# Optimization experiments

Hardware: AMD Instinct MI355X
Metric: run time of the kernel (lower is better)

Reference implementation:

```python
import jax, jax.numpy as jnp
import numpy as np

B, S, H, HEADS = 2, 2048, 1024, 16
KD = H // HEADS          # key_dim = 64
VDIM = 2 * H             # double_v_dim
HD = VDIM // HEADS       # head_size = 128
EPS = 1e-5


def _rotate_every_two(x):
    x1 = x[..., ::2]
    x2 = x[..., 1::2]
    return jnp.stack((-x2, x1), axis=-1).reshape(x.shape)


def _theta_shift(x, sin, cos):
    return x * cos + _rotate_every_two(x) * sin


def setup_inputs() -> dict:
    key = jax.random.key(0)
    ks = jax.random.split(key, 8)
    x = jax.random.normal(ks[0], (B, S, H), dtype=jnp.float32)
    # RoPE-style angles over key_dim, each frequency repeated twice
    half = jnp.arange(KD // 2, dtype=jnp.float32)
    angle = 1.0 / (10000.0 ** (half / (KD // 2)))
    angle = jnp.repeat(angle, 2)                      # [KD]
    pos = jnp.arange(S, dtype=jnp.float32)[:, None]   # [S,1]
    sin = jnp.sin(pos * angle[None, :])               # [S,KD]
    cos = jnp.cos(pos * angle[None, :])
    # per-head exponential decay mask (RetNet)
    decay = 1.0 - 2.0 ** (-5.0 - jnp.arange(HEADS, dtype=jnp.float32))  # [heads]
    i = jnp.arange(S, dtype=jnp.float32)[:, None]
    j = jnp.arange(S, dtype=jnp.float32)[None, :]
    diff = i - j                                       # [S,S]
    logd = jnp.log(decay)[:, None, None]               # [heads,1,1]
    mask = jnp.where(diff[None] >= 0, jnp.exp(logd * diff[None]), 0.0).astype(jnp.float32)
    gain = 0.02
    Wq = gain * jax.random.normal(ks[1], (H, H), dtype=jnp.float32)
    Wk = gain * jax.random.normal(ks[2], (H, H), dtype=jnp.float32)
    Wv = gain * jax.random.normal(ks[3], (VDIM, H), dtype=jnp.float32)
    Wg = gain * jax.random.normal(ks[4], (VDIM, H), dtype=jnp.float32)
    Wo = gain * jax.random.normal(ks[5], (H, VDIM), dtype=jnp.float32)
    return {"x": x, "sin": sin, "cos": cos, "mask": mask,
            "Wq": Wq, "Wk": Wk, "Wv": Wv, "Wg": Wg, "Wo": Wo}


def reference(x, sin, cos, mask, Wq, Wk, Wv, Wg, Wo):
    b, s, h = x.shape
    heads = mask.shape[0]
    kd = h // heads
    vdim = Wv.shape[0]
    hd = vdim // heads
    scaling = kd ** -0.5

    q = jnp.einsum('bsh,oh->bso', x, Wq)
    k = jnp.einsum('bsh,oh->bso', x, Wk) * scaling
    v = jnp.einsum('bsh,oh->bso', x, Wv)
    g = jnp.einsum('bsh,oh->bso', x, Wg)

    q = q.reshape(b, s, heads, kd).transpose(0, 2, 1, 3)  # [b,h,s,kd]
    k = k.reshape(b, s, heads, kd).transpose(0, 2, 1, 3)
    qr = _theta_shift(q, sin, cos)
    kr = _theta_shift(k, sin, cos)

    vr = v.reshape(b, s, heads, hd).transpose(0, 2, 1, 3)  # [b,h,s,hd]

    qk = jnp.einsum('bhsk,bhtk->bhst', qr, kr) * mask      # [b,h,s,s]
    denom = jnp.maximum(jnp.abs(jax.lax.stop_gradient(qk).sum(-1, keepdims=True)), 1.0)
    qk = qk / denom

    out = jnp.einsum('bhst,bhtd->bhsd', qk, vr)            # [b,h,s,hd]
    out = out.transpose(0, 2, 1, 3)                        # [b,s,h,hd]
    # RMSNorm over head_size, no affine, eps=1e-5
    out = out * jax.lax.rsqrt(jnp.mean(out * out, axis=-1, keepdims=True) + EPS)
    out = out.reshape(b, s, heads * hd)                    # [b,s,vdim]
    out = (g * jax.nn.sigmoid(g)) * out                    # swish gate
    return jnp.einsum('bsv,ov->bso', out, Wo)
```

## Files before the change

kernel.cpp:

```cpp
#include <hip/hip_runtime.h>

typedef _Float16 f16;
typedef _Float16 f16x2 __attribute__((ext_vector_type(2)));
typedef _Float16 f16x4 __attribute__((ext_vector_type(4)));
typedef _Float16 f16x8 __attribute__((ext_vector_type(8)));
typedef float f32x4 __attribute__((ext_vector_type(4)));

#define MFMA_16x16x32(a, b, c) __builtin_amdgcn_mfma_f32_16x16x32_f16((a), (b), (c), 0, 0, 0)


__device__ __forceinline__ void async_ld16(const void* g, void* l) {
  __builtin_amdgcn_global_load_lds((const __attribute__((address_space(1))) unsigned int*)g,
                                   (__attribute__((address_space(3))) unsigned int*)l,
                                   16, 0, 0);
}

__global__ void k_cast_all(const float* __restrict__ x, const float* __restrict__ Wq,
                           const float* __restrict__ Wk, const float* __restrict__ Wv,
                           const float* __restrict__ Wg, const float* __restrict__ Wo,
                           f16* __restrict__ xh, f16* __restrict__ W1h, f16* __restrict__ Woh) {
  size_t u = ((size_t)blockIdx.x * 256 + threadIdx.x) * 4;
  const float* src;
  f16* dst;
  float sc = 1.0f;
  if (u < 4194304) {
    src = x + u; dst = xh + u;
  } else if (u < 10485760) {
    size_t idx = u - 4194304;
    int row = (int)(idx >> 10), col = (int)(idx & 1023);
    if (row < 1024)      { src = Wq + (size_t)row * 1024 + col; }
    else if (row < 2048) { src = Wk + (size_t)(row - 1024) * 1024 + col; sc = 0.125f; }
    else if (row < 4096) { src = Wv + (size_t)(row - 2048) * 1024 + col; }
    else                 { src = Wg + (size_t)(row - 4096) * 1024 + col; }
    dst = W1h + idx;
  } else {
    size_t idx = u - 10485760;
    src = Wo + idx; dst = Woh + idx;
  }
  float4 v = *(const float4*)src;
  f16x4 r = { (f16)(v.x * sc), (f16)(v.y * sc), (f16)(v.z * sc), (f16)(v.w * sc) };
  *(f16x4*)dst = r;
}

template <int NT, typename OutT>
__global__ __launch_bounds__(256, 2)
void k_gemm_bt(const f16* __restrict__ A, const f16* __restrict__ Bw,
               OutT* __restrict__ C, int M, int N, int K) {
  __shared__ f16 As[128 * 64];
  __shared__ f16 Bs[NT * 64];
  constexpr int NR = NT / 16;
  const int tid = threadIdx.x;
  const int lane = tid & 63, w = tid >> 6;
  const int quad = lane >> 4, rm = lane & 15;
  const int mt = blockIdx.y, nt = blockIdx.x;
  const f16* Ab = A + (size_t)mt * 128 * K;
  const f16* Bb = Bw + (size_t)nt * NT * K;
  f32x4 acc[2][NR] = {};

  const int sr = lane >> 3;
  const int sc8 = (lane & 7) * 8;

  for (int k0 = 0; k0 < K; k0 += 64) {
    __syncthreads();
#pragma unroll
    for (int p = 0; p < 4; ++p) {
      int br = w * 32 + p * 8;
      async_ld16(Ab + (size_t)(br + sr) * K + k0 + sc8, &As[br * 64]);
    }
#pragma unroll
    for (int p = 0; p < NT / 32; ++p) {
      int br = w * (NT / 4) + p * 8;
      async_ld16(Bb + (size_t)(br + sr) * K + k0 + sc8, &Bs[br * 64]);
    }
    __syncthreads();
#pragma unroll
    for (int kk = 0; kk < 64; kk += 32) {
      const int ko = kk + quad * 8;
      f16x8 a0 = *(const f16x8*)(&As[(w * 32 + rm) * 64 + ko]);
      f16x8 a1 = *(const f16x8*)(&As[(w * 32 + 16 + rm) * 64 + ko]);
#pragma unroll
      for (int n = 0; n < NR; ++n) {
        f16x8 bf = *(const f16x8*)(&Bs[(n * 16 + rm) * 64 + ko]);
        acc[0][n] = MFMA_16x16x32(a0, bf, acc[0][n]);
        acc[1][n] = MFMA_16x16x32(a1, bf, acc[1][n]);
      }
    }
  }
#pragma unroll
  for (int m = 0; m < 2; ++m)
#pragma unroll
    for (int n = 0; n < NR; ++n)
#pragma unroll
      for (int r = 0; r < 4; ++r) {
        int row = mt * 128 + w * 32 + m * 16 + quad * 4 + r;
        int col = nt * NT + n * 16 + rm;
        C[(size_t)row * N + col] = (OutT)acc[m][n][r];
      }
}

__global__ void k_rope(f16* __restrict__ qkvg, const float* __restrict__ sinp,
                       const float* __restrict__ cosp) {
  int u = blockIdx.x * 256 + threadIdx.x;
  int row = u >> 10;
  int col = (u & 1023) * 2;
  int s = row & 2047;
  int d = col & 63;
  f16x2* p = (f16x2*)(qkvg + (size_t)row * 6144 + col);
  f16x2 xv = *p;
  float xe = (float)xv[0], xo = (float)xv[1];
  float se = sinp[s * 64 + d], so = sinp[s * 64 + d + 1];
  float ce = cosp[s * 64 + d], co = cosp[s * 64 + d + 1];
  f16x2 r = { (f16)(xe * ce - xo * se), (f16)(xo * co + xe * so) };
  *p = r;
}

__device__ __forceinline__ int off136(int d) { return d * 136 + ((d >> 3) << 3); }

__global__ __launch_bounds__(256, 2)
void k_state(const f16* __restrict__ qkvg, float* __restrict__ Sws, float* __restrict__ skws) {
  __shared__ f16 Kt[8752];
  __shared__ f16 Vt[17520];
  __shared__ float skbuf[4][64];
  const int tid = threadIdx.x;
  const int lane = tid & 63, w = tid >> 6;
  const int quad = lane >> 4, rm = lane & 15;
  const int c = blockIdx.x, h = blockIdx.y, b = blockIdx.z;
  const int bh = b * 16 + h;
  const size_t ld = 6144;
  const f16* base = qkvg + (size_t)b * 2048 * ld + (size_t)c * 128 * ld;
  const float logd = logf(1.0f - exp2f(-5.0f - (float)h));

#pragma unroll
  for (int p = 0; p < 4; ++p) {
    int tau = p * 32 + (tid >> 3);
    int kd0 = (tid & 7) * 8;
    f16x8 kv = *(const f16x8*)(base + (size_t)tau * ld + 1024 + h * 64 + kd0);
    float g = expf(logd * (float)(127 - tau));
#pragma unroll
    for (int j = 0; j < 8; ++j) Kt[off136(kd0 + j) + tau] = (f16)((float)kv[j] * g);
  }
#pragma unroll
  for (int p = 0; p < 8; ++p) {
    int tau = p * 16 + (tid >> 4);
    int d0 = (tid & 15) * 8;
    f16x8 vv = *(const f16x8*)(base + (size_t)tau * ld + 2048 + h * 128 + d0);
#pragma unroll
    for (int j = 0; j < 8; ++j) Vt[off136(d0 + j) + tau] = vv[j];
  }
  __syncthreads();

  f32x4 acc[2][4] = {};
#pragma unroll
  for (int kf = 0; kf < 4; ++kf) {
    int k0 = kf * 32 + quad * 8;
    f16x8 av[2];
#pragma unroll
    for (int mm = 0; mm < 2; ++mm)
      av[mm] = *(const f16x8*)(&Vt[off136(w * 32 + mm * 16 + rm) + k0]);
#pragma unroll
    for (int n = 0; n < 4; ++n) {
      f16x8 bk = *(const f16x8*)(&Kt[off136(n * 16 + rm) + k0]);
#pragma unroll
      for (int mm = 0; mm < 2; ++mm) acc[mm][n] = MFMA_16x16x32(av[mm], bk, acc[mm][n]);
    }
  }
  float* Sout = Sws + ((size_t)c * 32 + bh) * 8192;
#pragma unroll
  for (int mm = 0; mm < 2; ++mm)
#pragma unroll
    for (int n = 0; n < 4; ++n)
#pragma unroll
      for (int r = 0; r < 4; ++r)
        Sout[(w * 32 + mm * 16 + quad * 4 + r) * 64 + n * 16 + rm] = acc[mm][n][r];

  {
    int kd = tid & 63;
    float p = 0.f;
    for (int tau = w * 32; tau < w * 32 + 32; ++tau) p += (float)Kt[off136(kd) + tau];
    skbuf[w][kd] = p;
  }
  __syncthreads();
  if (tid < 64) {
    float s = skbuf[0][tid] + skbuf[1][tid] + skbuf[2][tid] + skbuf[3][tid];
    skws[((size_t)c * 32 + bh) * 64 + tid] = s;
  }
}

__global__ __launch_bounds__(256, 2)
void k_scan(const float* __restrict__ Sws, const float* __restrict__ skws,
            f16* __restrict__ Rtws, float* __restrict__ rktws) {
  const int bh = blockIdx.x;
  const int h = bh & 15;
  const int tid = threadIdx.x;
  const float logd = logf(1.0f - exp2f(-5.0f - (float)h));
  const float gC = expf(logd * 128.0f);
  float R[32];
#pragma unroll
  for (int i = 0; i < 32; ++i) R[i] = 0.f;
  float rk = 0.f;
  for (int c = 0; c < 16; ++c) {
    size_t bs = ((size_t)c * 32 + bh) * 8192;
    f16* rt = Rtws + bs;
    const float* sp = Sws + bs;
#pragma unroll
    for (int i = 0; i < 32; ++i) {
      rt[tid * 32 + i] = (f16)R[i];
      R[i] = gC * R[i] + sp[tid * 32 + i];
    }
    if (tid < 64) {
      size_t ks = ((size_t)c * 32 + bh) * 64 + tid;
      rktws[ks] = rk;
      rk = gC * rk + skws[ks];
    }
  }
}

__device__ __forceinline__ int vt_off(int d) { return d * 40 + (d >> 3) * 8; }

__global__ __launch_bounds__(256, 4)
void k_attn(const f16* __restrict__ qkvg, const f16* __restrict__ Rtws,
            const float* __restrict__ rktws, f16* __restrict__ act) {
  constexpr int LDK = 72;
  constexpr int LDP = 40;
  __shared__ f16 Ks[32 * LDK];
  __shared__ f16 Vt[5240];
  __shared__ f16 Ps[4][16 * LDP];
  const int tid = threadIdx.x;
  const int lane = tid & 63, w = tid >> 6;
  const int quad = lane >> 4, rm = lane & 15;
  int bx = blockIdx.x;
  if (blockIdx.z) bx = 31 - bx;
  const int h = blockIdx.y, b = blockIdx.z;
  const int bh = b * 16 + h;
  const int s_blk = bx * 64;
  const int c = s_blk >> 7;
  const size_t ld = 6144;
  const f16* base = qkvg + (size_t)b * 2048 * ld;
  const float logd = logf(1.0f - exp2f(-5.0f - (float)h));

  f16x8 qa[2];
  {
    int row = s_blk + w * 16 + rm;
#pragma unroll
    for (int kh = 0; kh < 2; ++kh)
      qa[kh] = *(const f16x8*)(base + (size_t)row * ld + h * 64 + kh * 32 + quad * 8);
  }
  int voff[8];
#pragma unroll
  for (int n = 0; n < 8; ++n) voff[n] = vt_off(n * 16 + rm) + quad * 8;

  f32x4 od[8];
#pragma unroll
  for (int n = 0; n < 8; ++n) od[n] = (f32x4){0.f, 0.f, 0.f, 0.f};
  float den[4] = {0.f, 0.f, 0.f, 0.f};

  const int tmax = s_blk + 64;
  for (int t0 = c * 128; t0 < tmax; t0 += 32) {
    __syncthreads();
    {
      int r = tid >> 3, cc = (tid & 7) * 8;
      *(uint4*)(&Ks[r * LDK + cc]) =
          *(const uint4*)(base + (size_t)(t0 + r) * ld + 1024 + h * 64 + cc);
    }
#pragma unroll
    for (int p = 0; p < 2; ++p) {
      int t = p * 16 + (tid >> 4);
      int d0 = (tid & 15) * 8;
      f16x8 v = *(const f16x8*)(base + (size_t)(t0 + t) * ld + 2048 + h * 128 + d0);
#pragma unroll
      for (int j = 0; j < 8; ++j) Vt[vt_off(d0 + j) + t] = v[j];
    }
    __syncthreads();

    f32x4 st[2];
#pragma unroll
    for (int ts = 0; ts < 2; ++ts) st[ts] = (f32x4){0.f, 0.f, 0.f, 0.f};
#pragma unroll
    for (int ts = 0; ts < 2; ++ts) {
      f16x8 bk0 = *(const f16x8*)(&Ks[(ts * 16 + rm) * LDK + quad * 8]);
      f16x8 bk1 = *(const f16x8*)(&Ks[(ts * 16 + rm) * LDK + 32 + quad * 8]);
      st[ts] = MFMA_16x16x32(qa[0], bk0, st[ts]);
      st[ts] = MFMA_16x16x32(qa[1], bk1, st[ts]);
    }
#pragma unroll
    for (int ts = 0; ts < 2; ++ts)
#pragma unroll
      for (int r = 0; r < 4; ++r) {
        int s = s_blk + w * 16 + quad * 4 + r;
        int t = t0 + ts * 16 + rm;
        int diff = s - t;
        float pv = 0.f;
        if (diff >= 0) pv = st[ts][r] * expf(logd * (float)diff);
        den[r] += pv;
        Ps[w][(quad * 4 + r) * LDP + ts * 16 + rm] = (f16)pv;
      }
    __syncthreads();
    f16x8 pa = *(const f16x8*)(&Ps[w][rm * LDP + quad * 8]);
#pragma unroll
    for (int n = 0; n < 8; ++n) {
      f16x8 bv = *(const f16x8*)(&Vt[voff[n]]);
      od[n] = MFMA_16x16x32(pa, bv, od[n]);
    }
  }

  {
    const f16* Rt = Rtws + ((size_t)c * 32 + bh) * 8192;
    float g1 = expf(logd * (float)(s_blk - c * 128 + w * 16 + rm + 1));
    f16x8 qg[2];
#pragma unroll
    for (int kh = 0; kh < 2; ++kh)
#pragma unroll
      for (int j = 0; j < 8; ++j) qg[kh][j] = (f16)((float)qa[kh][j] * g1);
#pragma unroll
    for (int n = 0; n < 8; ++n) {
      f16x8 b0 = *(const f16x8*)(Rt + (size_t)(n * 16 + rm) * 64 + quad * 8);
      f16x8 b1 = *(const f16x8*)(Rt + (size_t)(n * 16 + rm) * 64 + 32 + quad * 8);
      od[n] = MFMA_16x16x32(qg[0], b0, od[n]);
      od[n] = MFMA_16x16x32(qg[1], b1, od[n]);
    }
    const float* rkp = rktws + ((size_t)c * 32 + bh) * 64;
    f16x8 bd0, bd1;
#pragma unroll
    for (int j = 0; j < 8; ++j) {
      bd0[j] = (rm == 0) ? (f16)rkp[quad * 8 + j] : (f16)0.f;
      bd1[j] = (rm == 0) ? (f16)rkp[32 + quad * 8 + j] : (f16)0.f;
    }
    f32x4 sd = (f32x4){0.f, 0.f, 0.f, 0.f};
    sd = MFMA_16x16x32(qg[0], bd0, sd);
    sd = MFMA_16x16x32(qg[1], bd1, sd);
#pragma unroll
    for (int r = 0; r < 4; ++r) den[r] += sd[r];
  }

  float dn[4], rr[4];
#pragma unroll
  for (int r = 0; r < 4; ++r) {
    float d = den[r];
    d += __shfl_xor(d, 1, 16);
    d += __shfl_xor(d, 2, 16);
    d += __shfl_xor(d, 4, 16);
    d += __shfl_xor(d, 8, 16);
    dn[r] = fmaxf(fabsf(d), 1.0f);
  }
  float ssq[4] = {0.f, 0.f, 0.f, 0.f};
#pragma unroll
  for (int n = 0; n < 8; ++n)
#pragma unroll
    for (int r = 0; r < 4; ++r) {
      float o = od[n][r] / dn[r];
      od[n][r] = o;
      ssq[r] += o * o;
    }
#pragma unroll
  for (int r = 0; r < 4; ++r) {
    float s2 = ssq[r];
    s2 += __shfl_xor(s2, 1, 16);
    s2 += __shfl_xor(s2, 2, 16);
    s2 += __shfl_xor(s2, 4, 16);
    s2 += __shfl_xor(s2, 8, 16);
    rr[r] = rsqrtf(s2 * (1.0f / 128.0f) + 1e-5f);
  }
#pragma unroll
  for (int n = 0; n < 8; ++n)
#pragma unroll
    for (int r = 0; r < 4; ++r) {
      int s = s_blk + w * 16 + quad * 4 + r;
      int dcol = n * 16 + rm;
      float g = (float)base[(size_t)s * ld + 4096 + h * 128 + dcol];
      float o = od[n][r] * rr[r];
      float a = (g / (1.0f + expf(-g))) * o;
      act[((size_t)b * 2048 + s) * 2048 + h * 128 + dcol] = (f16)a;
    }
}

extern "C" void kernel_launch(void* const* d_in, const int* in_sizes, int n_in,
                              void* d_out, int out_size, void* d_ws, size_t ws_size,
                              hipStream_t stream) {
  const float* x    = (const float*)d_in[0];
  const float* sinp = (const float*)d_in[1];
  const float* cosp = (const float*)d_in[2];
  const float* Wq = (const float*)d_in[4];
  const float* Wk = (const float*)d_in[5];
  const float* Wv = (const float*)d_in[6];
  const float* Wg = (const float*)d_in[7];
  const float* Wo = (const float*)d_in[8];
  float* out = (float*)d_out;

  char* ws = (char*)d_ws;
  f16* xh     = (f16*)(ws);
  f16* W1h    = (f16*)(ws + 8388608);
  f16* Woh    = (f16*)(ws + 20971520);
  f16* qkvg   = (f16*)(ws + 25165824);
  f16* acth   = (f16*)(ws + 75497472);
  float* Sws  = (float*)(ws + 92274688);
  f16* Rtws   = (f16*)(ws + 109051904);
  float* skws = (float*)(ws + 117440512);
  float* rktws= (float*)(ws + 117571584);

  k_cast_all<<<12288, 256, 0, stream>>>(x, Wq, Wk, Wv, Wg, Wo, xh, W1h, Woh);

  k_gemm_bt<128, f16><<<dim3(48, 32), 256, 0, stream>>>(xh, W1h, qkvg, 4096, 6144, 1024);

  k_rope<<<16384, 256, 0, stream>>>(qkvg, sinp, cosp);

  k_state<<<dim3(16, 16, 2), 256, 0, stream>>>(qkvg, Sws, skws);
  k_scan<<<32, 256, 0, stream>>>(Sws, skws, Rtws, rktws);
  k_attn<<<dim3(32, 16, 2), 256, 0, stream>>>(qkvg, Rtws, rktws, acth);

  k_gemm_bt<64, float><<<dim3(16, 32), 256, 0, stream>>>(acth, Woh, out, 4096, 1024, 2048);
}
```

Measured before the change: 518.8 us.

## Fuse RoPE into QKVG GEMM epilogue, store chunk states in fp16, parallelize scan

Applies the rotary shift inside the projection GEMM epilogue, pairing adjacent columns with a lane shuffle, and removes the separate k_rope pass over q and k. Chunk state matrices are written in fp16 instead of fp32, which halves that workspace traffic. The scan kernel is split across 8 slabs per batch-head with vectorized 4-wide accesses instead of 32 sequential values per thread, giving 256 blocks rather than 32. The costs are some precision loss in the stored states and extra sin/cos loads in the GEMM epilogue.

Measured after the change: 499.2 us. 3.8% less time.

```diff
diff --git a/kernel.cpp b/kernel.cpp
--- a/kernel.cpp
+++ b/kernel.cpp
@@ -42,10 +42,11 @@
   *(f16x4*)dst = r;
 }
 
-template <int NT, typename OutT>
+template <int NT, bool ROPE, typename OutT>
 __global__ __launch_bounds__(256, 2)
 void k_gemm_bt(const f16* __restrict__ A, const f16* __restrict__ Bw,
-               OutT* __restrict__ C, int M, int N, int K) {
+               OutT* __restrict__ C, const float* __restrict__ sinp,
+               const float* __restrict__ cosp, int M, int N, int K) {
   __shared__ f16 As[128 * 64];
   __shared__ f16 Bs[NT * 64];
   constexpr int NR = NT / 16;
@@ -86,6 +87,7 @@
       }
     }
   }
+  const bool rope_tile = ROPE && (nt * NT < 2048);
 #pragma unroll
   for (int m = 0; m < 2; ++m)
 #pragma unroll
@@ -94,30 +96,22 @@
       for (int r = 0; r < 4; ++r) {
         int row = mt * 128 + w * 32 + m * 16 + quad * 4 + r;
         int col = nt * NT + n * 16 + rm;
-        C[(size_t)row * N + col] = (OutT)acc[m][n][r];
+        float val = acc[m][n][r];
+        if (rope_tile) {
+          float par = __shfl_xor(val, 1);
+          int s = row & 2047;
+          int d = col & 63;
+          float sv = sinp[s * 64 + d], cv = cosp[s * 64 + d];
+          val = (col & 1) ? (val * cv + par * sv) : (val * cv - par * sv);
+        }
+        C[(size_t)row * N + col] = (OutT)val;
       }
 }
 
-__global__ void k_rope(f16* __restrict__ qkvg, const float* __restrict__ sinp,
-                       const float* __restrict__ cosp) {
-  int u = blockIdx.x * 256 + threadIdx.x;
-  int row = u >> 10;
-  int col = (u & 1023) * 2;
-  int s = row & 2047;
-  int d = col & 63;
-  f16x2* p = (f16x2*)(qkvg + (size_t)row * 6144 + col);
-  f16x2 xv = *p;
-  float xe = (float)xv[0], xo = (float)xv[1];
-  float se = sinp[s * 64 + d], so = sinp[s * 64 + d + 1];
-  float ce = cosp[s * 64 + d], co = cosp[s * 64 + d + 1];
-  f16x2 r = { (f16)(xe * ce - xo * se), (f16)(xo * co + xe * so) };
-  *p = r;
-}
-
 __device__ __forceinline__ int off136(int d) { return d * 136 + ((d >> 3) << 3); }
 
 __global__ __launch_bounds__(256, 2)
-void k_state(const f16* __restrict__ qkvg, float* __restrict__ Sws, float* __restrict__ skws) {
+void k_state(const f16* __restrict__ qkvg, f16* __restrict__ Sws, float* __restrict__ skws) {
   __shared__ f16 Kt[8752];
   __shared__ f16 Vt[17520];
   __shared__ float skbuf[4][64];
@@ -164,14 +158,14 @@
       for (int mm = 0; mm < 2; ++mm) acc[mm][n] = MFMA_16x16x32(av[mm], bk, acc[mm][n]);
     }
   }
-  float* Sout = Sws + ((size_t)c * 32 + bh) * 8192;
+  f16* Sout = Sws + ((size_t)c * 32 + bh) * 8192;
 #pragma unroll
   for (int mm = 0; mm < 2; ++mm)
 #pragma unroll
     for (int n = 0; n < 4; ++n)
 #pragma unroll
       for (int r = 0; r < 4; ++r)
-        Sout[(w * 32 + mm * 16 + quad * 4 + r) * 64 + n * 16 + rm] = acc[mm][n][r];
+        Sout[(w * 32 + mm * 16 + quad * 4 + r) * 64 + n * 16 + rm] = (f16)acc[mm][n][r];
 
   {
     int kd = tid & 63;
@@ -187,27 +181,27 @@
 }
 
 __global__ __launch_bounds__(256, 2)
-void k_scan(const float* __restrict__ Sws, const float* __restrict__ skws,
+void k_scan(const f16* __restrict__ Sws, const float* __restrict__ skws,
             f16* __restrict__ Rtws, float* __restrict__ rktws) {
   const int bh = blockIdx.x;
+  const int slab = blockIdx.y;
   const int h = bh & 15;
   const int tid = threadIdx.x;
   const float logd = logf(1.0f - exp2f(-5.0f - (float)h));
   const float gC = expf(logd * 128.0f);
-  float R[32];
-#pragma unroll
-  for (int i = 0; i < 32; ++i) R[i] = 0.f;
-  float rk = 0.f;
+  const int idx = slab * 1024 + tid * 4;
+  float R[4] = {0.f, 0.f, 0.f, 0.f};
   for (int c = 0; c < 16; ++c) {
-    size_t bs = ((size_t)c * 32 + bh) * 8192;
-    f16* rt = Rtws + bs;
-    const float* sp = Sws + bs;
-#pragma unroll
-    for (int i = 0; i < 32; ++i) {
-      rt[tid * 32 + i] = (f16)R[i];
-      R[i] = gC * R[i] + sp[tid * 32 + i];
-    }
-    if (tid < 64) {
+    size_t bs = ((size_t)c * 32 + bh) * 8192 + idx;
+    f16x4 rv = { (f16)R[0], (f16)R[1], (f16)R[2], (f16)R[3] };
+    *(f16x4*)(Rtws + bs) = rv;
+    f16x4 sv = *(const f16x4*)(Sws + bs);
+#pragma unroll
+    for (int i = 0; i < 4; ++i) R[i] = gC * R[i] + (float)sv[i];
+  }
+  if (slab == 0 && tid < 64) {
+    float rk = 0.f;
+    for (int c = 0; c < 16; ++c) {
       size_t ks = ((size_t)c * 32 + bh) * 64 + tid;
       rktws[ks] = rk;
       rk = gC * rk + skws[ks];
@@ -392,20 +386,20 @@
   f16* Woh    = (f16*)(ws + 20971520);
   f16* qkvg   = (f16*)(ws + 25165824);
   f16* acth   = (f16*)(ws + 75497472);
-  float* Sws  = (float*)(ws + 92274688);
-  f16* Rtws   = (f16*)(ws + 109051904);
-  float* skws = (float*)(ws + 117440512);
-  float* rktws= (float*)(ws + 117571584);
+  f16* Sws    = (f16*)(ws + 92274688);
+  f16* Rtws   = (f16*)(ws + 100663296);
+  float* skws = (float*)(ws + 109051904);
+  float* rktws= (float*)(ws + 109182976);
 
   k_cast_all<<<12288, 256, 0, stream>>>(x, Wq, Wk, Wv, Wg, Wo, xh, W1h, Woh);
 
-  k_gemm_bt<128, f16><<<dim3(48, 32), 256, 0, stream>>>(xh, W1h, qkvg, 4096, 6144, 1024);
-
-  k_rope<<<16384, 256, 0, stream>>>(qkvg, sinp, cosp);
+  k_gemm_bt<128, true, f16><<<dim3(48, 32), 256, 0, stream>>>(
+      xh, W1h, qkvg, sinp, cosp, 4096, 6144, 1024);
 
   k_state<<<dim3(16, 16, 2), 256, 0, stream>>>(qkvg, Sws, skws);
-  k_scan<<<32, 256, 0, stream>>>(Sws, skws, Rtws, rktws);
+  k_scan<<<dim3(32, 8), 256, 0, stream>>>(Sws, skws, Rtws, rktws);
   k_attn<<<dim3(32, 16, 2), 256, 0, stream>>>(qkvg, Rtws, rktws, acth);
 
-  k_gemm_bt<64, float><<<dim3(16, 32), 256, 0, stream>>>(acth, Woh, out, 4096, 1024, 2048);
-}
+  k_gemm_bt<64, false, float><<<dim3(16, 32), 256, 0, stream>>>(
+      acth, Woh, out, nullptr, nullptr, 4096, 1024, 2048);
+}
```
